# Optimization experiments

Hardware: AMD Instinct MI355X
Metric: run time of the kernel (lower is better)

## Reference

```python
import jax, jax.numpy as jnp
import numpy as np

B, L, D, Y = 8, 2500, 512, 8921


def setup_inputs() -> dict:
    key = jax.random.key(0)
    k1, k2, k3, k4, k5, k6 = jax.random.split(key, 6)
    x = jax.random.normal(k1, (B, L, D), dtype=jnp.float32)
    target = jax.random.uniform(k2, (B, Y), dtype=jnp.float32)
    text_inputs = jax.random.randint(k3, (B, L), 0, 50000, dtype=jnp.int32)
    # Xavier-uniform-like init for the two [Y, D] weights
    lim = float(np.sqrt(6.0 / (Y + D)))
    U_weight = jax.random.uniform(k4, (Y, D), dtype=jnp.float32, minval=-lim, maxval=lim)
    final_weight = jax.random.uniform(k5, (Y, D), dtype=jnp.float32, minval=-lim, maxval=lim)
    final_bias = jax.random.uniform(k6, (Y,), dtype=jnp.float32, minval=-0.05, maxval=0.05)
    return {"x": x, "target": target, "text_inputs": text_inputs,
            "U_weight": U_weight, "final_weight": final_weight, "final_bias": final_bias}


def reference(x, target, text_inputs, U_weight, final_weight, final_bias):
    # att: [B, Y, L] = U.weight @ x^T
    att = jnp.einsum('yd,bld->byl', U_weight, x)
    # softmax over sequence dim
    alpha = jax.nn.softmax(att, axis=2)
    # per-label context: [B, Y, D]
    m = jnp.einsum('byl,bld->byd', alpha, x)
    # gated reduction instead of a linear layer: [B, Y]
    y = jnp.einsum('byd,yd->by', m, final_weight) + final_bias
    # BCEWithLogitsLoss (mean over all elements), numerically stable
    loss = jnp.mean(jnp.maximum(y, 0.0) - y * target + jnp.log1p(jnp.exp(-jnp.abs(y))))
    return (y, loss)
```

## Files before the change

### kernel.cpp

```cpp
#include <hip/hip_runtime.h>
#include <stdint.h>

#define B_ 8
#define L_ 2500
#define D_ 512
#define Y_ 8921
#define LP 2560
#define YP 8960
#define BLK 128
#define BK 32
#define NKT 16
#define NS 4
#define LTS 5

typedef float f32x4 __attribute__((ext_vector_type(4)));
typedef __bf16 bf16x8 __attribute__((ext_vector_type(8)));
typedef unsigned short u16;
typedef unsigned int u32;

__device__ __forceinline__ u32 pack2(float a, float b) {
  u32 ua = __float_as_uint(a); ua = (ua + 0x7FFFu + ((ua >> 16) & 1u)) >> 16;
  u32 ub = __float_as_uint(b); ub = (ub + 0x7FFFu + ((ub >> 16) & 1u)) >> 16;
  return ua | (ub << 16);
}

__global__ void cvt_x_kernel(const float* __restrict__ x, u16* __restrict__ xb) {
  int idx = blockIdx.x * 256 + threadIdx.x;
  int row = idx >> 6;
  int c8  = (idx & 63) << 3;
  int b = row / LP;
  int l = row - b * LP;
  uint4 o;
  if (l < L_) {
    const float* s = x + (size_t)(b * L_ + l) * D_ + c8;
    float4 f0 = *(const float4*)s;
    float4 f1 = *(const float4*)(s + 4);
    o.x = pack2(f0.x, f0.y); o.y = pack2(f0.z, f0.w);
    o.z = pack2(f1.x, f1.y); o.w = pack2(f1.z, f1.w);
  } else {
    o = make_uint4(0u, 0u, 0u, 0u);
  }
  *(uint4*)(xb + (size_t)row * D_ + c8) = o;
}

__global__ void cvt_w_kernel(const float* __restrict__ U, const float* __restrict__ Wf,
                             u16* __restrict__ Ub, u16* __restrict__ Wb) {
  int idx = blockIdx.x * 256 + threadIdx.x;
  const int half = YP * 64;
  const float* src = U; u16* dst = Ub;
  int i = idx;
  if (idx >= half) { i -= half; src = Wf; dst = Wb; }
  int row = i >> 6;
  int c8  = (i & 63) << 3;
  uint4 o;
  if (row < Y_) {
    const float* s = src + (size_t)row * D_ + c8;
    float4 f0 = *(const float4*)s;
    float4 f1 = *(const float4*)(s + 4);
    o.x = pack2(f0.x, f0.y); o.y = pack2(f0.z, f0.w);
    o.z = pack2(f1.x, f1.y); o.w = pack2(f1.z, f1.w);
  } else {
    o = make_uint4(0u, 0u, 0u, 0u);
  }
  *(uint4*)(dst + (size_t)row * D_ + c8) = o;
}

__device__ __forceinline__ void async16(const u16* g, u16* l) {
  __builtin_amdgcn_global_load_lds(
      (const __attribute__((address_space(1))) u32*)g,
      (__attribute__((address_space(3))) u32*)l, 16, 0, 0);
}

__global__ __launch_bounds__(256, 3) void fused_kernel(
    const u16* __restrict__ xb,
    const u16* __restrict__ Ub,
    const u16* __restrict__ Wb,
    float* __restrict__ part)
{
  __shared__ __align__(16) u16 sU[BLK * BK];
  __shared__ __align__(16) u16 sW[BLK * BK];
  __shared__ __align__(16) u16 sX[BLK * BK];

  const int t    = threadIdx.x;
  const int lane = t & 63;
  const int wv   = t >> 6;
  const int l16  = lane & 15;
  const int q    = lane >> 4;
  const int b    = blockIdx.y;
  const int y0   = blockIdx.x * BLK;
  const int s    = blockIdx.z;

  const int srow = t >> 2;
  const int scol = (t & 3) << 3;
  const u16* gU0 = Ub + (size_t)(y0 + srow) * D_ + scol;
  const u16* gW0 = Wb + (size_t)(y0 + srow) * D_ + scol;
  const u16* gXb = xb + (size_t)b * LP * D_ + (size_t)srow * D_ + scol;
  u16* lU0 = sU + t * 8;
  u16* lW0 = sW + t * 8;
  u16* lX0 = sX + t * 8;

  float Z[8], W[8];
#pragma unroll
  for (int i = 0; i < 8; ++i) { Z[i] = 0.f; W[i] = 0.f; }

  const f32x4 z4 = {0.f, 0.f, 0.f, 0.f};

  for (int ltl = 0; ltl < LTS; ++ltl) {
    const int l0 = (s * LTS + ltl) * BLK;
    const u16* gX0 = gXb + (size_t)l0 * D_;

    f32x4 accA[2][8], accS[2][8];
#pragma unroll
    for (int ry = 0; ry < 2; ++ry)
#pragma unroll
      for (int cl = 0; cl < 8; ++cl) { accA[ry][cl] = z4; accS[ry][cl] = z4; }

    for (int kt = 0; kt < NKT; ++kt) {
      const int ko = kt * BK;
      __syncthreads();
      async16(gU0 + ko, lU0);
      async16(gU0 + ko + (size_t)64 * D_, lU0 + 2048);
      async16(gW0 + ko, lW0);
      async16(gW0 + ko + (size_t)64 * D_, lW0 + 2048);
      async16(gX0 + ko, lX0);
      async16(gX0 + ko + (size_t)64 * D_, lX0 + 2048);
      __syncthreads();

      bf16x8 aU0 = *(const bf16x8*)(const void*)(sU + (wv * 32 + l16) * BK + q * 8);
      bf16x8 aU1 = *(const bf16x8*)(const void*)(sU + (wv * 32 + 16 + l16) * BK + q * 8);
      bf16x8 aW0 = *(const bf16x8*)(const void*)(sW + (wv * 32 + l16) * BK + q * 8);
      bf16x8 aW1 = *(const bf16x8*)(const void*)(sW + (wv * 32 + 16 + l16) * BK + q * 8);
#pragma unroll
      for (int cl = 0; cl < 8; ++cl) {
        bf16x8 bX = *(const bf16x8*)(const void*)(sX + (cl * 16 + l16) * BK + q * 8);
        accA[0][cl] = __builtin_amdgcn_mfma_f32_16x16x32_bf16(aU0, bX, accA[0][cl], 0, 0, 0);
        accA[1][cl] = __builtin_amdgcn_mfma_f32_16x16x32_bf16(aU1, bX, accA[1][cl], 0, 0, 0);
        accS[0][cl] = __builtin_amdgcn_mfma_f32_16x16x32_bf16(aW0, bX, accS[0][cl], 0, 0, 0);
        accS[1][cl] = __builtin_amdgcn_mfma_f32_16x16x32_bf16(aW1, bX, accS[1][cl], 0, 0, 0);
      }
    }

    const bool boundary = (l0 + BLK > L_);
#pragma unroll
    for (int ry = 0; ry < 2; ++ry) {
#pragma unroll
      for (int r = 0; r < 4; ++r) {
        const int si = ry * 4 + r;
        float zl = 0.f, wl = 0.f;
        if (boundary) {
#pragma unroll
          for (int cl = 0; cl < 8; ++cl) {
            float v = accA[ry][cl][r];
            if (l0 + cl * 16 + l16 >= L_) v = -1e30f;
            const float p = __expf(v);
            zl += p;
            wl = fmaf(p, accS[ry][cl][r], wl);
          }
        } else {
#pragma unroll
          for (int cl = 0; cl < 8; ++cl) {
            const float p = __expf(accA[ry][cl][r]);
            zl += p;
            wl = fmaf(p, accS[ry][cl][r], wl);
          }
        }
        Z[si] += zl;
        W[si] += wl;
      }
    }
  }

#pragma unroll
  for (int si = 0; si < 8; ++si) {
    float Z0 = Z[si], W0 = W[si];
#pragma unroll
    for (int st = 1; st <= 8; st <<= 1) {
      Z0 += __shfl_xor(Z0, st);
      W0 += __shfl_xor(W0, st);
    }
    Z[si] = Z0; W[si] = W0;
  }

  if (l16 == 0) {
    float* p = part + ((size_t)(b * 70 + blockIdx.x) * NS + s) * 256;
#pragma unroll
    for (int ry = 0; ry < 2; ++ry) {
#pragma unroll
      for (int r = 0; r < 4; ++r) {
        const int si = ry * 4 + r;
        const int yl = wv * 32 + ry * 16 + q * 4 + r;
        p[yl]       = Z[si];
        p[128 + yl] = W[si];
      }
    }
  }
}

__global__ void combine_kernel(const float* __restrict__ part,
                               const float* __restrict__ bias,
                               const float* __restrict__ target,
                               float* __restrict__ out) {
  const int idx = blockIdx.x * 256 + threadIdx.x;
  float lpart = 0.f;
  if (idx < B_ * Y_) {
    const int b = idx / Y_;
    const int y = idx - b * Y_;
    const int yt = y >> 7, yl = y & 127;
    const float* p = part + ((size_t)(b * 70 + yt) * NS) * 256 + yl;
    float Z = 0.f, W = 0.f;
#pragma unroll
    for (int s2 = 0; s2 < NS; ++s2) {
      Z += p[s2 * 256];
      W += p[s2 * 256 + 128];
    }
    const float yv = W / Z + bias[y];
    out[idx] = yv;
    const float tg = target[idx];
    lpart = fmaxf(yv, 0.f) - yv * tg + log1pf(__expf(-fabsf(yv)));
  }
  lpart += __shfl_xor(lpart, 1);  lpart += __shfl_xor(lpart, 2);
  lpart += __shfl_xor(lpart, 4);  lpart += __shfl_xor(lpart, 8);
  lpart += __shfl_xor(lpart, 16); lpart += __shfl_xor(lpart, 32);
  if ((threadIdx.x & 63) == 0)
    atomicAdd(out + (size_t)B_ * Y_, lpart * (1.0f / (B_ * Y_)));
}

extern "C" void kernel_launch(void* const* d_in, const int* in_sizes, int n_in,
                              void* d_out, int out_size, void* d_ws, size_t ws_size,
                              hipStream_t stream) {
  const float* x      = (const float*)d_in[0];
  const float* target = (const float*)d_in[1];
  const float* U      = (const float*)d_in[3];
  const float* Wf     = (const float*)d_in[4];
  const float* bias   = (const float*)d_in[5];
  float* out = (float*)d_out;

  u16* xb = (u16*)d_ws;
  u16* Ub = xb + (size_t)B_ * LP * D_;
  u16* Wb = Ub + (size_t)YP * D_;
  float* part = (float*)(Wb + (size_t)YP * D_);

  hipMemsetAsync(out + (size_t)B_ * Y_, 0, sizeof(float), stream);
  cvt_x_kernel<<<dim3((B_ * LP * 64) / 256), 256, 0, stream>>>(x, xb);
  cvt_w_kernel<<<dim3((2 * YP * 64) / 256), 256, 0, stream>>>(U, Wf, Ub, Wb);
  fused_kernel<<<dim3(YP / BLK, B_, NS), 256, 0, stream>>>(xb, Ub, Wb, part);
  combine_kernel<<<dim3((B_ * Y_ + 255) / 256), 256, 0, stream>>>(part, bias, target, out);
}
```

Before: 575.3 us.

## Use 32x32 MFMA with pre-packed weight fragments loaded directly from global

The weights U and Wf are repacked into an MFMA-fragment-ordered layout, so each wave loads its A operands straight from global memory instead of staging them through LDS. Only the x tile stays in shared memory, now with an XOR swizzle to avoid bank conflicts. The inner product switches from 16x16x32 to 32x32x16 MFMA. This is meant to cut LDS traffic and the number of barriers' worth of loads per tile, at the cost of uncached per-wave global loads on the critical path and higher register use, with launch bounds lowered to 2 blocks per SIMD.

```diff
diff --git a/kernel.cpp b/kernel.cpp
--- a/kernel.cpp
+++ b/kernel.cpp
@@ -8,12 +8,12 @@
 #define LP 2560
 #define YP 8960
 #define BLK 128
-#define BK 32
 #define NKT 16
 #define NS 4
 #define LTS 5
-
-typedef float f32x4 __attribute__((ext_vector_type(4)));
+#define YT32 280
+
+typedef float  f32x16 __attribute__((ext_vector_type(16)));
 typedef __bf16 bf16x8 __attribute__((ext_vector_type(8)));
 typedef unsigned short u16;
 typedef unsigned int u32;
@@ -43,26 +43,29 @@
   *(uint4*)(xb + (size_t)row * D_ + c8) = o;
 }
 
-__global__ void cvt_w_kernel(const float* __restrict__ U, const float* __restrict__ Wf,
-                             u16* __restrict__ Ub, u16* __restrict__ Wb) {
-  int idx = blockIdx.x * 256 + threadIdx.x;
-  const int half = YP * 64;
-  const float* src = U; u16* dst = Ub;
-  int i = idx;
-  if (idx >= half) { i -= half; src = Wf; dst = Wb; }
-  int row = i >> 6;
-  int c8  = (i & 63) << 3;
+__global__ void cvt_wpk_kernel(const float* __restrict__ U, const float* __restrict__ Wf,
+                               u16* __restrict__ Upk, u16* __restrict__ Wpk) {
+  int gid = blockIdx.x * 256 + threadIdx.x;
+  const int half = YT32 * 32 * 64;
+  const float* src = U; u16* dst = Upk;
+  int i = gid;
+  if (gid >= half) { i -= half; src = Wf; dst = Wpk; }
+  const int lane = i & 63;
+  const int ks   = (i >> 6) & 31;
+  const int yt   = i >> 11;
+  const int y    = yt * 32 + (lane & 31);
+  const int k    = ks * 16 + (lane >> 5) * 8;
   uint4 o;
-  if (row < Y_) {
-    const float* s = src + (size_t)row * D_ + c8;
-    float4 f0 = *(const float4*)s;
-    float4 f1 = *(const float4*)(s + 4);
+  if (y < Y_) {
+    const float* sp = src + (size_t)y * D_ + k;
+    float4 f0 = *(const float4*)sp;
+    float4 f1 = *(const float4*)(sp + 4);
     o.x = pack2(f0.x, f0.y); o.y = pack2(f0.z, f0.w);
     o.z = pack2(f1.x, f1.y); o.w = pack2(f1.z, f1.w);
   } else {
     o = make_uint4(0u, 0u, 0u, 0u);
   }
-  *(uint4*)(dst + (size_t)row * D_ + c8) = o;
+  *(uint4*)(dst + (size_t)i * 8) = o;
 }
 
 __device__ __forceinline__ void async16(const u16* g, u16* l) {
@@ -71,127 +74,101 @@
       (__attribute__((address_space(3))) u32*)l, 16, 0, 0);
 }
 
-__global__ __launch_bounds__(256, 3) void fused_kernel(
+__global__ __launch_bounds__(256, 2) void fused_kernel(
     const u16* __restrict__ xb,
-    const u16* __restrict__ Ub,
-    const u16* __restrict__ Wb,
+    const u16* __restrict__ Upk,
+    const u16* __restrict__ Wpk,
     float* __restrict__ part)
 {
-  __shared__ __align__(16) u16 sU[BLK * BK];
-  __shared__ __align__(16) u16 sW[BLK * BK];
-  __shared__ __align__(16) u16 sX[BLK * BK];
+  __shared__ __align__(16) u16 sX[128 * 32];
 
   const int t    = threadIdx.x;
   const int lane = t & 63;
   const int wv   = t >> 6;
-  const int l16  = lane & 15;
-  const int q    = lane >> 4;
+  const int c32  = lane & 31;
+  const int h    = lane >> 5;
   const int b    = blockIdx.y;
-  const int y0   = blockIdx.x * BLK;
   const int s    = blockIdx.z;
+  const int yt32 = blockIdx.x * 4 + wv;
+
+  const u16* pU = Upk + (size_t)yt32 * 16384 + lane * 8;
+  const u16* pW = Wpk + (size_t)yt32 * 16384 + lane * 8;
 
   const int srow = t >> 2;
-  const int scol = (t & 3) << 3;
-  const u16* gU0 = Ub + (size_t)(y0 + srow) * D_ + scol;
-  const u16* gW0 = Wb + (size_t)(y0 + srow) * D_ + scol;
-  const u16* gXb = xb + (size_t)b * LP * D_ + (size_t)srow * D_ + scol;
-  u16* lU0 = sU + t * 8;
-  u16* lW0 = sW + t * 8;
-  u16* lX0 = sX + t * 8;
-
-  float Z[8], W[8];
-#pragma unroll
-  for (int i = 0; i < 8; ++i) { Z[i] = 0.f; W[i] = 0.f; }
-
-  const f32x4 z4 = {0.f, 0.f, 0.f, 0.f};
+  const int gch  = (t & 3) ^ (srow & 3);
+  const u16* gXb = xb + ((size_t)b * LP + srow) * 512 + gch * 8;
+
+  float Zr[16], Wr[16];
+#pragma unroll
+  for (int i = 0; i < 16; ++i) { Zr[i] = 0.f; Wr[i] = 0.f; }
 
   for (int ltl = 0; ltl < LTS; ++ltl) {
     const int l0 = (s * LTS + ltl) * BLK;
-    const u16* gX0 = gXb + (size_t)l0 * D_;
-
-    f32x4 accA[2][8], accS[2][8];
-#pragma unroll
-    for (int ry = 0; ry < 2; ++ry)
-#pragma unroll
-      for (int cl = 0; cl < 8; ++cl) { accA[ry][cl] = z4; accS[ry][cl] = z4; }
+    const u16* gX = gXb + (size_t)l0 * 512;
+
+    f32x16 accA[4], accS[4];
+#pragma unroll
+    for (int cl = 0; cl < 4; ++cl) {
+      accA[cl] = (f32x16)(0.f);
+      accS[cl] = (f32x16)(0.f);
+    }
 
     for (int kt = 0; kt < NKT; ++kt) {
-      const int ko = kt * BK;
       __syncthreads();
-      async16(gU0 + ko, lU0);
-      async16(gU0 + ko + (size_t)64 * D_, lU0 + 2048);
-      async16(gW0 + ko, lW0);
-      async16(gW0 + ko + (size_t)64 * D_, lW0 + 2048);
-      async16(gX0 + ko, lX0);
-      async16(gX0 + ko + (size_t)64 * D_, lX0 + 2048);
+      async16(gX + kt * 32,             sX + t * 8);
+      async16(gX + kt * 32 + 64 * 512,  sX + 2048 + t * 8);
       __syncthreads();
 
-      bf16x8 aU0 = *(const bf16x8*)(const void*)(sU + (wv * 32 + l16) * BK + q * 8);
-      bf16x8 aU1 = *(const bf16x8*)(const void*)(sU + (wv * 32 + 16 + l16) * BK + q * 8);
-      bf16x8 aW0 = *(const bf16x8*)(const void*)(sW + (wv * 32 + l16) * BK + q * 8);
-      bf16x8 aW1 = *(const bf16x8*)(const void*)(sW + (wv * 32 + 16 + l16) * BK + q * 8);
-#pragma unroll
-      for (int cl = 0; cl < 8; ++cl) {
-        bf16x8 bX = *(const bf16x8*)(const void*)(sX + (cl * 16 + l16) * BK + q * 8);
-        accA[0][cl] = __builtin_amdgcn_mfma_f32_16x16x32_bf16(aU0, bX, accA[0][cl], 0, 0, 0);
-        accA[1][cl] = __builtin_amdgcn_mfma_f32_16x16x32_bf16(aU1, bX, accA[1][cl], 0, 0, 0);
-        accS[0][cl] = __builtin_amdgcn_mfma_f32_16x16x32_bf16(aW0, bX, accS[0][cl], 0, 0, 0);
-        accS[1][cl] = __builtin_amdgcn_mfma_f32_16x16x32_bf16(aW1, bX, accS[1][cl], 0, 0, 0);
+      const bf16x8 aU0 = *(const bf16x8*)(const void*)(pU + kt * 1024);
+      const bf16x8 aU1 = *(const bf16x8*)(const void*)(pU + kt * 1024 + 512);
+      const bf16x8 aW0 = *(const bf16x8*)(const void*)(pW + kt * 1024);
+      const bf16x8 aW1 = *(const bf16x8*)(const void*)(pW + kt * 1024 + 512);
+#pragma unroll
+      for (int cl = 0; cl < 4; ++cl) {
+        const int r  = cl * 32 + c32;
+        const int sw = r & 3;
+        const bf16x8 b0 = *(const bf16x8*)(const void*)(sX + r * 32 + ((h     ^ sw) << 3));
+        const bf16x8 b1 = *(const bf16x8*)(const void*)(sX + r * 32 + (((2+h) ^ sw) << 3));
+        accA[cl] = __builtin_amdgcn_mfma_f32_32x32x16_bf16(aU0, b0, accA[cl], 0, 0, 0);
+        accA[cl] = __builtin_amdgcn_mfma_f32_32x32x16_bf16(aU1, b1, accA[cl], 0, 0, 0);
+        accS[cl] = __builtin_amdgcn_mfma_f32_32x32x16_bf16(aW0, b0, accS[cl], 0, 0, 0);
+        accS[cl] = __builtin_amdgcn_mfma_f32_32x32x16_bf16(aW1, b1, accS[cl], 0, 0, 0);
       }
     }
 
     const bool boundary = (l0 + BLK > L_);
 #pragma unroll
-    for (int ry = 0; ry < 2; ++ry) {
-#pragma unroll
-      for (int r = 0; r < 4; ++r) {
-        const int si = ry * 4 + r;
-        float zl = 0.f, wl = 0.f;
-        if (boundary) {
-#pragma unroll
-          for (int cl = 0; cl < 8; ++cl) {
-            float v = accA[ry][cl][r];
-            if (l0 + cl * 16 + l16 >= L_) v = -1e30f;
-            const float p = __expf(v);
-            zl += p;
-            wl = fmaf(p, accS[ry][cl][r], wl);
-          }
-        } else {
-#pragma unroll
-          for (int cl = 0; cl < 8; ++cl) {
-            const float p = __expf(accA[ry][cl][r]);
-            zl += p;
-            wl = fmaf(p, accS[ry][cl][r], wl);
-          }
-        }
-        Z[si] += zl;
-        W[si] += wl;
+    for (int cl = 0; cl < 4; ++cl) {
+      const bool dead = boundary && (l0 + cl * 32 + c32 >= L_);
+#pragma unroll
+      for (int reg = 0; reg < 16; ++reg) {
+        float v = accA[cl][reg];
+        if (dead) v = -1e30f;
+        const float p = __expf(v);
+        Zr[reg] += p;
+        Wr[reg] = fmaf(p, accS[cl][reg], Wr[reg]);
       }
     }
   }
 
 #pragma unroll
-  for (int si = 0; si < 8; ++si) {
-    float Z0 = Z[si], W0 = W[si];
-#pragma unroll
-    for (int st = 1; st <= 8; st <<= 1) {
+  for (int reg = 0; reg < 16; ++reg) {
+    float Z0 = Zr[reg], W0 = Wr[reg];
+#pragma unroll
+    for (int st = 1; st <= 16; st <<= 1) {
       Z0 += __shfl_xor(Z0, st);
       W0 += __shfl_xor(W0, st);
     }
-    Z[si] = Z0; W[si] = W0;
-  }
-
-  if (l16 == 0) {
+    Zr[reg] = Z0; Wr[reg] = W0;
+  }
+
+  if (c32 == 0) {
     float* p = part + ((size_t)(b * 70 + blockIdx.x) * NS + s) * 256;
 #pragma unroll
-    for (int ry = 0; ry < 2; ++ry) {
-#pragma unroll
-      for (int r = 0; r < 4; ++r) {
-        const int si = ry * 4 + r;
-        const int yl = wv * 32 + ry * 16 + q * 4 + r;
-        p[yl]       = Z[si];
-        p[128 + yl] = W[si];
-      }
+    for (int reg = 0; reg < 16; ++reg) {
+      const int yl = wv * 32 + (reg & 3) + 8 * (reg >> 2) + 4 * h;
+      p[yl]       = Zr[reg];
+      p[128 + yl] = Wr[reg];
     }
   }
 }
@@ -235,14 +212,14 @@
   const float* bias   = (const float*)d_in[5];
   float* out = (float*)d_out;
 
-  u16* xb = (u16*)d_ws;
-  u16* Ub = xb + (size_t)B_ * LP * D_;
-  u16* Wb = Ub + (size_t)YP * D_;
-  float* part = (float*)(Wb + (size_t)YP * D_);
+  u16* xb  = (u16*)d_ws;
+  u16* Upk = xb + (size_t)B_ * LP * D_;
+  u16* Wpk = Upk + (size_t)YT32 * 32 * 512;
+  float* part = (float*)(Wpk + (size_t)YT32 * 32 * 512);
 
   hipMemsetAsync(out + (size_t)B_ * Y_, 0, sizeof(float), stream);
   cvt_x_kernel<<<dim3((B_ * LP * 64) / 256), 256, 0, stream>>>(x, xb);
-  cvt_w_kernel<<<dim3((2 * YP * 64) / 256), 256, 0, stream>>>(U, Wf, Ub, Wb);
-  fused_kernel<<<dim3(YP / BLK, B_, NS), 256, 0, stream>>>(xb, Ub, Wb, part);
+  cvt_wpk_kernel<<<dim3((2 * YT32 * 32 * 64) / 256), 256, 0, stream>>>(U, Wf, Upk, Wpk);
+  fused_kernel<<<dim3(YP / BLK, B_, NS), 256, 0, stream>>>(xb, Upk, Wpk, part);
   combine_kernel<<<dim3((B_ * Y_ + 255) / 256), 256, 0, stream>>>(part, bias, target, out);
 }
```

Result: no change. 577.1 us (+0.3%).
